# Optimization experiments

Measured on AMD Instinct MI355X. Metric: run time of the kernel, lower is better.

The kernel has to match this reference:

```python
import jax, jax.numpy as jnp
import numpy as np

TOKENS = 1024
IN_W = 512
BLOCK = 256
OUT_W = 512
N_BLOCKS = 64
K = 2


def setup_inputs() -> dict:
    key = jax.random.key(0)
    ks = jax.random.split(key, 8)
    u = lambda k, s: jax.random.uniform(k, s, jnp.float32, -1.0, 1.0)
    return {
        "x": jax.random.normal(ks[0], (TOKENS, IN_W), jnp.float32),
        "noise": jax.random.normal(ks[1], (TOKENS, N_BLOCKS), jnp.float32),
        "w1s": u(ks[2], (N_BLOCKS, IN_W, BLOCK)),
        "b1s": u(ks[3], (N_BLOCKS, BLOCK)),
        "w2s": u(ks[4], (N_BLOCKS, BLOCK, OUT_W)),
        "b2s": u(ks[5], (N_BLOCKS, OUT_W)),
        "mixer": jnp.zeros((IN_W, N_BLOCKS), jnp.float32) + 0.01 * jax.random.normal(ks[6], (IN_W, N_BLOCKS), jnp.float32),
        "noise_controller": jnp.zeros((IN_W, N_BLOCKS), jnp.float32) + 0.01 * jax.random.normal(ks[7], (IN_W, N_BLOCKS), jnp.float32),
        "k": K,
    }


def reference(x, noise, w1s, b1s, w2s, b2s, mixer, noise_controller, k):
    # noisy routing logits: mixer_prod + randn * softplus(noise_prod)
    h_x = x @ mixer + noise * jax.nn.softplus(x @ noise_controller)  # [B, E]
    topk_vals, topk_idx = jax.lax.top_k(h_x, k)                       # [B, K]
    scores = jax.nn.softmax(topk_vals, axis=-1)                       # [B, K]
    # per-token expert weight gather (faithful to index_select semantics)
    gw1 = w1s[topk_idx]  # [B, K, I, H]
    gb1 = b1s[topk_idx]  # [B, K, H]
    gw2 = w2s[topk_idx]  # [B, K, H, O]
    gb2 = b2s[topk_idx]  # [B, K, O]
    v = jax.nn.relu(jnp.einsum('bi,bkih->bkh', x, gw1) + gb1)        # [B, K, H]
    out = jnp.einsum('bkh,bkho->bko', v, gw2) + gb2                   # [B, K, O]
    return jnp.sum(out * scores[..., None], axis=1)                   # [B, O]
```

## Files before the change

kernel.cpp:

```cpp
#include <hip/hip_runtime.h>
#include <math.h>

#define TOKENS    1024
#define IN_W      512
#define BLOCK_H   256
#define OUT_W     512
#define N_EXPERTS 64
#define TOPK      2
#define NSLOTS    (TOKENS * TOPK)
#define LIST_CAP  128
#define T_GRP     12
#define NGRP      4
#define XPAD      520
#define OSPAD     516
#define VPAD      264

__global__ __launch_bounds__(256) void routing_kernel(
    const float* __restrict__ x, const float* __restrict__ noise,
    const float* __restrict__ mixer, const float* __restrict__ noisec,
    float* __restrict__ esc, int* __restrict__ counts, int* __restrict__ lists)
{
    __shared__ float xs[2 * 512];
    __shared__ float pm[2 * 2 * 64];
    __shared__ float pn[2 * 2 * 64];
    const int blk  = blockIdx.x;
    const int tid  = threadIdx.x;
    const int wave = tid >> 6, lane = tid & 63;
    const int tq = wave >> 1;
    const int ih = wave & 1;

    ((float4*)xs)[tid] = ((const float4*)x)[(size_t)blk * 256 + tid];
    __syncthreads();

    float am = 0.f, an = 0.f;
    const float* xp = xs + tq * 512 + ih * 256;
    const float* mp = mixer  + (size_t)(ih * 256) * 64 + lane;
    const float* np = noisec + (size_t)(ih * 256) * 64 + lane;
    #pragma unroll 8
    for (int i = 0; i < 256; ++i) {
        const float xv = xp[i];
        am = fmaf(xv, mp[i * 64], am);
        an = fmaf(xv, np[i * 64], an);
    }
    pm[tq * 128 + ih * 64 + lane] = am;
    pn[tq * 128 + ih * 64 + lane] = an;
    __syncthreads();

    if (tid < 128) {
        const int e = tid & 63, tt = tid >> 6;
        const int t = blk * 2 + tt;
        const float am2 = pm[tt * 128 + e] + pm[tt * 128 + 64 + e];
        const float an2 = pn[tt * 128 + e] + pn[tt * 128 + 64 + e];
        const float sp = fmaxf(an2, 0.f) + log1pf(expf(-fabsf(an2)));
        pm[tt * 128 + e] = am2 + noise[(size_t)t * 64 + e] * sp;
    }
    __syncthreads();

    if (tid < 2) {
        const float* h = pm + tid * 128;
        float b0 = -INFINITY, b1 = -INFINITY;
        int i0 = 0, i1 = 0;
        for (int i = 0; i < N_EXPERTS; ++i) {
            const float v = h[i];
            if (v > b0)      { b1 = b0; i1 = i0; b0 = v; i0 = i; }
            else if (v > b1) { b1 = v; i1 = i; }
        }
        const float z   = expf(b1 - b0);
        const float inv = 1.f / (1.f + z);
        const int t = blk * 2 + tid;
        esc[t * 2 + 0] = inv;
        esc[t * 2 + 1] = z * inv;
        const int p0 = atomicAdd(&counts[i0], 1);
        if (p0 < LIST_CAP) lists[i0 * LIST_CAP + p0] = t * 2 + 0;
        const int p1 = atomicAdd(&counts[i1], 1);
        if (p1 < LIST_CAP) lists[i1 * LIST_CAP + p1] = t * 2 + 1;
    }
}

__global__ __launch_bounds__(1024, 4) void expert_kernel(
    const float* __restrict__ x,
    const float* __restrict__ w1s, const float* __restrict__ b1s,
    const float* __restrict__ w2s, const float* __restrict__ b2s,
    const int* __restrict__ counts, const int* __restrict__ lists,
    const float* __restrict__ esc, float* __restrict__ out)
{
    __shared__ __align__(16) float smem[T_GRP * XPAD];
    __shared__ __align__(16) float vsm[T_GRP * VPAD];
    __shared__ int   slotIds[T_GRP];
    __shared__ float escv[T_GRP];

    const int e  = blockIdx.x;
    const int g  = blockIdx.y;
    const int ne = min(counts[e], LIST_CAP);
    const int tid  = threadIdx.x;
    const int wave = tid >> 6, lane = tid & 63;

    const int cq1  = wave & 3;
    const int tt   = wave >> 2;
    const int c4_1 = cq1 * 16 + (lane & 15);
    const int r1   = lane >> 4;
    const int c4_2 = cq1 * 32 + (lane & 31);
    const int r2   = lane >> 5;
    const int t0   = tt * 3;

    const float4* w1v = (const float4*)(w1s + (size_t)e * IN_W * BLOCK_H);
    const float4* w2v = (const float4*)(w2s + (size_t)e * BLOCK_H * OUT_W);
    const float4* b1v = (const float4*)(b1s + (size_t)e * BLOCK_H);
    const float4* b2v = (const float4*)(b2s + (size_t)e * OUT_W);
    const float4* x4  = (const float4*)x;

    for (int base = g * T_GRP; base < ne; base += NGRP * T_GRP) {
        const int nTok = min(T_GRP, ne - base);
        if (tid < T_GRP) {
            const int s = (tid < nTok) ? lists[e * LIST_CAP + base + tid] : 0;
            slotIds[tid] = s;
            escv[tid]    = esc[s];
        }
        __syncthreads();

        for (int idx = tid; idx < T_GRP * 128; idx += 1024) {
            const int t = idx >> 7, q = idx & 127;
            float4 v = make_float4(0.f, 0.f, 0.f, 0.f);
            if (t < nTok) v = x4[(size_t)(slotIds[t] >> 1) * 128 + q];
            *(float4*)&smem[t * XPAD + q * 4] = v;
        }
        __syncthreads();

        float4 a0 = make_float4(0.f, 0.f, 0.f, 0.f), a1 = a0, a2 = a0;
        {
            const float4* wp = w1v + (size_t)(r1 * 64 + c4_1);
            const float* xb0 = smem + (t0 + 0) * XPAD + r1;
            const float* xb1 = smem + (t0 + 1) * XPAD + r1;
            const float* xb2 = smem + (t0 + 2) * XPAD + r1;
            #pragma unroll 4
            for (int i = 0; i < IN_W; i += 4) {
                const float4 w = wp[(size_t)i * 64];
                const float xv0 = xb0[i], xv1 = xb1[i], xv2 = xb2[i];
                a0.x = fmaf(xv0, w.x, a0.x); a0.y = fmaf(xv0, w.y, a0.y);
                a0.z = fmaf(xv0, w.z, a0.z); a0.w = fmaf(xv0, w.w, a0.w);
                a1.x = fmaf(xv1, w.x, a1.x); a1.y = fmaf(xv1, w.y, a1.y);
                a1.z = fmaf(xv1, w.z, a1.z); a1.w = fmaf(xv1, w.w, a1.w);
                a2.x = fmaf(xv2, w.x, a2.x); a2.y = fmaf(xv2, w.y, a2.y);
                a2.z = fmaf(xv2, w.z, a2.z); a2.w = fmaf(xv2, w.w, a2.w);
            }
        }
        #pragma unroll
        for (int m = 16; m <= 32; m <<= 1) {
            a0.x += __shfl_xor(a0.x, m); a0.y += __shfl_xor(a0.y, m);
            a0.z += __shfl_xor(a0.z, m); a0.w += __shfl_xor(a0.w, m);
            a1.x += __shfl_xor(a1.x, m); a1.y += __shfl_xor(a1.y, m);
            a1.z += __shfl_xor(a1.z, m); a1.w += __shfl_xor(a1.w, m);
            a2.x += __shfl_xor(a2.x, m); a2.y += __shfl_xor(a2.y, m);
            a2.z += __shfl_xor(a2.z, m); a2.w += __shfl_xor(a2.w, m);
        }
        if (lane < 16) {
            const float4 bb = b1v[c4_1];
            float4 r;
            r.x = fmaxf(a0.x + bb.x, 0.f); r.y = fmaxf(a0.y + bb.y, 0.f);
            r.z = fmaxf(a0.z + bb.z, 0.f); r.w = fmaxf(a0.w + bb.w, 0.f);
            *(float4*)&vsm[(t0 + 0) * VPAD + c4_1 * 4] = r;
            r.x = fmaxf(a1.x + bb.x, 0.f); r.y = fmaxf(a1.y + bb.y, 0.f);
            r.z = fmaxf(a1.z + bb.z, 0.f); r.w = fmaxf(a1.w + bb.w, 0.f);
            *(float4*)&vsm[(t0 + 1) * VPAD + c4_1 * 4] = r;
            r.x = fmaxf(a2.x + bb.x, 0.f); r.y = fmaxf(a2.y + bb.y, 0.f);
            r.z = fmaxf(a2.z + bb.z, 0.f); r.w = fmaxf(a2.w + bb.w, 0.f);
            *(float4*)&vsm[(t0 + 2) * VPAD + c4_1 * 4] = r;
        }
        __syncthreads();

        float4 o0 = make_float4(0.f, 0.f, 0.f, 0.f), o1 = o0, o2 = o0;
        {
            const float4* wp2 = w2v + (size_t)(r2 * 128 + c4_2);
            const float* vb0 = vsm + (t0 + 0) * VPAD + r2;
            const float* vb1 = vsm + (t0 + 1) * VPAD + r2;
            const float* vb2 = vsm + (t0 + 2) * VPAD + r2;
            #pragma unroll 4
            for (int h = 0; h < BLOCK_H; h += 2) {
                const float4 w = wp2[(size_t)h * 128];
                const float v0 = vb0[h], v1 = vb1[h], v2 = vb2[h];
                o0.x = fmaf(v0, w.x, o0.x); o0.y = fmaf(v0, w.y, o0.y);
                o0.z = fmaf(v0, w.z, o0.z); o0.w = fmaf(v0, w.w, o0.w);
                o1.x = fmaf(v1, w.x, o1.x); o1.y = fmaf(v1, w.y, o1.y);
                o1.z = fmaf(v1, w.z, o1.z); o1.w = fmaf(v1, w.w, o1.w);
                o2.x = fmaf(v2, w.x, o2.x); o2.y = fmaf(v2, w.y, o2.y);
                o2.z = fmaf(v2, w.z, o2.z); o2.w = fmaf(v2, w.w, o2.w);
            }
        }
        o0.x += __shfl_xor(o0.x, 32); o0.y += __shfl_xor(o0.y, 32);
        o0.z += __shfl_xor(o0.z, 32); o0.w += __shfl_xor(o0.w, 32);
        o1.x += __shfl_xor(o1.x, 32); o1.y += __shfl_xor(o1.y, 32);
        o1.z += __shfl_xor(o1.z, 32); o1.w += __shfl_xor(o1.w, 32);
        o2.x += __shfl_xor(o2.x, 32); o2.y += __shfl_xor(o2.y, 32);
        o2.z += __shfl_xor(o2.z, 32); o2.w += __shfl_xor(o2.w, 32);
        if (lane < 32) {
            *(float4*)&smem[(t0 + 0) * OSPAD + c4_2 * 4] = o0;
            *(float4*)&smem[(t0 + 1) * OSPAD + c4_2 * 4] = o1;
            *(float4*)&smem[(t0 + 2) * OSPAD + c4_2 * 4] = o2;
        }
        __syncthreads();

        for (int idx = tid; idx < T_GRP * 128; idx += 1024) {
            const int t = idx >> 7, q = idx & 127;
            if (t < nTok) {
                const float4 r  = *(const float4*)&smem[t * OSPAD + q * 4];
                const float4 bb = b2v[q];
                const float  sc = escv[t];
                float* o = out + (size_t)(slotIds[t] >> 1) * OUT_W + q * 4;
                atomicAdd(o + 0, (r.x + bb.x) * sc);
                atomicAdd(o + 1, (r.y + bb.y) * sc);
                atomicAdd(o + 2, (r.z + bb.z) * sc);
                atomicAdd(o + 3, (r.w + bb.w) * sc);
            }
        }
        __syncthreads();
    }
}

extern "C" void kernel_launch(void* const* d_in, const int* in_sizes, int n_in,
                              void* d_out, int out_size, void* d_ws, size_t ws_size,
                              hipStream_t stream) {
    const float* x      = (const float*)d_in[0];
    const float* noise  = (const float*)d_in[1];
    const float* w1s    = (const float*)d_in[2];
    const float* b1s    = (const float*)d_in[3];
    const float* w2s    = (const float*)d_in[4];
    const float* b2s    = (const float*)d_in[5];
    const float* mixer  = (const float*)d_in[6];
    const float* noisec = (const float*)d_in[7];
    float* out = (float*)d_out;

    char* ws = (char*)d_ws;
    int*   counts = (int*)ws;                       ws += 256;
    float* esc    = (float*)ws;                     ws += NSLOTS * sizeof(float);
    int*   lists  = (int*)ws;

    hipMemsetAsync(d_out, 0, (size_t)out_size * sizeof(float), stream);
    hipMemsetAsync(counts, 0, 256, stream);

    routing_kernel<<<TOKENS / 2, 256, 0, stream>>>(x, noise, mixer, noisec,
                                                   esc, counts, lists);
    expert_kernel<<<dim3(N_EXPERTS, NGRP), 1024, 0, stream>>>(
        x, w1s, b1s, w2s, b2s, counts, lists, esc, out);
}
```

Measured before the change: 180.7 us.

## Make each wave compute all tokens per expert pass, with templated token-count paths

Each wave now owns a slice of output columns and accumulates every token in the group, so each weight element is loaded once per block instead of once per token-triple wave group. Tokens are interleaved across the NGRP blocks so load is balanced. A template on token count (4/8/12) trims wasted FMAs and staging for sparse experts. The second GEMM's reduced results go straight to global atomics, dropping the output shared-memory stage and one barrier. Larger per-thread accumulator arrays raise register pressure and may lower occupancy.

```diff
diff --git a/kernel.cpp b/kernel.cpp
--- a/kernel.cpp
+++ b/kernel.cpp
@@ -9,10 +9,9 @@
 #define TOPK      2
 #define NSLOTS    (TOKENS * TOPK)
 #define LIST_CAP  128
-#define T_GRP     12
+#define T_CAP     12
 #define NGRP      4
 #define XPAD      520
-#define OSPAD     516
 #define VPAD      264
 
 __global__ __launch_bounds__(256) void routing_kernel(
@@ -77,6 +76,98 @@
     }
 }
 
+__device__ __forceinline__ void red_xor(float4& v, int m) {
+    v.x += __shfl_xor(v.x, m); v.y += __shfl_xor(v.y, m);
+    v.z += __shfl_xor(v.z, m); v.w += __shfl_xor(v.w, m);
+}
+
+template<int T>
+__device__ __forceinline__ void run_pass(
+    int nTok, int wave, int lane,
+    const float4* __restrict__ w1v, const float4* __restrict__ w2v,
+    const float4* __restrict__ b1v, const float4* __restrict__ b2v,
+    const float* __restrict__ xs, float* __restrict__ vsm,
+    const int* __restrict__ slotIds, const float* __restrict__ escv,
+    float* __restrict__ out)
+{
+    {
+        const int c4l = lane & 3, r0 = lane >> 2;
+        float4 acc[T];
+        #pragma unroll
+        for (int t = 0; t < T; ++t) acc[t] = make_float4(0.f, 0.f, 0.f, 0.f);
+        const float4* wp = w1v + (size_t)(r0 * 64 + wave * 4 + c4l);
+        const float*  xb = xs + r0;
+        #pragma unroll 2
+        for (int s = 0; s < 32; ++s) {
+            const float4 w = wp[(size_t)s * 1024];
+            #pragma unroll
+            for (int t = 0; t < T; ++t) {
+                const float xv = xb[t * XPAD + s * 16];
+                acc[t].x = fmaf(xv, w.x, acc[t].x);
+                acc[t].y = fmaf(xv, w.y, acc[t].y);
+                acc[t].z = fmaf(xv, w.z, acc[t].z);
+                acc[t].w = fmaf(xv, w.w, acc[t].w);
+            }
+        }
+        #pragma unroll
+        for (int t = 0; t < T; ++t) {
+            red_xor(acc[t], 4); red_xor(acc[t], 8);
+            red_xor(acc[t], 16); red_xor(acc[t], 32);
+        }
+        if (r0 == 0) {
+            const float4 bb = b1v[wave * 4 + c4l];
+            #pragma unroll
+            for (int t = 0; t < T; ++t) {
+                float4 r;
+                r.x = fmaxf(acc[t].x + bb.x, 0.f);
+                r.y = fmaxf(acc[t].y + bb.y, 0.f);
+                r.z = fmaxf(acc[t].z + bb.z, 0.f);
+                r.w = fmaxf(acc[t].w + bb.w, 0.f);
+                *(float4*)&vsm[t * VPAD + wave * 16 + c4l * 4] = r;
+            }
+        }
+    }
+    __syncthreads();
+
+    {
+        const int c8 = lane & 7, r8 = lane >> 3;
+        float4 acc[T];
+        #pragma unroll
+        for (int t = 0; t < T; ++t) acc[t] = make_float4(0.f, 0.f, 0.f, 0.f);
+        const float4* wp = w2v + (size_t)(r8 * 128 + wave * 8 + c8);
+        const float*  vb = vsm + r8;
+        #pragma unroll 2
+        for (int s = 0; s < 32; ++s) {
+            const float4 w = wp[(size_t)s * 1024];
+            #pragma unroll
+            for (int t = 0; t < T; ++t) {
+                const float vv = vb[t * VPAD + s * 8];
+                acc[t].x = fmaf(vv, w.x, acc[t].x);
+                acc[t].y = fmaf(vv, w.y, acc[t].y);
+                acc[t].z = fmaf(vv, w.z, acc[t].z);
+                acc[t].w = fmaf(vv, w.w, acc[t].w);
+            }
+        }
+        #pragma unroll
+        for (int t = 0; t < T; ++t) {
+            red_xor(acc[t], 8); red_xor(acc[t], 16); red_xor(acc[t], 32);
+        }
+        const float4 bb = b2v[wave * 8 + c8];
+        #pragma unroll
+        for (int t = 0; t < T; ++t) {
+            if ((t & 7) == r8 && t < nTok) {
+                const float sc = escv[t];
+                float* o = out + (size_t)(slotIds[t] >> 1) * OUT_W
+                               + (wave * 8 + c8) * 4;
+                atomicAdd(o + 0, (acc[t].x + bb.x) * sc);
+                atomicAdd(o + 1, (acc[t].y + bb.y) * sc);
+                atomicAdd(o + 2, (acc[t].z + bb.z) * sc);
+                atomicAdd(o + 3, (acc[t].w + bb.w) * sc);
+            }
+        }
+    }
+}
+
 __global__ __launch_bounds__(1024, 4) void expert_kernel(
     const float* __restrict__ x,
     const float* __restrict__ w1s, const float* __restrict__ b1s,
@@ -84,10 +175,10 @@
     const int* __restrict__ counts, const int* __restrict__ lists,
     const float* __restrict__ esc, float* __restrict__ out)
 {
-    __shared__ __align__(16) float smem[T_GRP * XPAD];
-    __shared__ __align__(16) float vsm[T_GRP * VPAD];
-    __shared__ int   slotIds[T_GRP];
-    __shared__ float escv[T_GRP];
+    __shared__ __align__(16) float xs[T_CAP * XPAD];
+    __shared__ __align__(16) float vsm[T_CAP * VPAD];
+    __shared__ int   slotIds[T_CAP];
+    __shared__ float escv[T_CAP];
 
     const int e  = blockIdx.x;
     const int g  = blockIdx.y;
@@ -95,123 +186,38 @@
     const int tid  = threadIdx.x;
     const int wave = tid >> 6, lane = tid & 63;
 
-    const int cq1  = wave & 3;
-    const int tt   = wave >> 2;
-    const int c4_1 = cq1 * 16 + (lane & 15);
-    const int r1   = lane >> 4;
-    const int c4_2 = cq1 * 32 + (lane & 31);
-    const int r2   = lane >> 5;
-    const int t0   = tt * 3;
-
     const float4* w1v = (const float4*)(w1s + (size_t)e * IN_W * BLOCK_H);
     const float4* w2v = (const float4*)(w2s + (size_t)e * BLOCK_H * OUT_W);
     const float4* b1v = (const float4*)(b1s + (size_t)e * BLOCK_H);
     const float4* b2v = (const float4*)(b2s + (size_t)e * OUT_W);
     const float4* x4  = (const float4*)x;
 
-    for (int base = g * T_GRP; base < ne; base += NGRP * T_GRP) {
-        const int nTok = min(T_GRP, ne - base);
-        if (tid < T_GRP) {
-            const int s = (tid < nTok) ? lists[e * LIST_CAP + base + tid] : 0;
+    for (int s0 = g; s0 < ne; s0 += NGRP * T_CAP) {
+        const int nTok  = min(T_CAP, (ne - s0 + NGRP - 1) / NGRP);
+        const int Tpath = (nTok <= 4) ? 4 : (nTok <= 8) ? 8 : 12;
+
+        if (tid < T_CAP) {
+            int s = 0; float sc = 0.f;
+            if (tid < nTok) { s = lists[e * LIST_CAP + s0 + tid * NGRP]; sc = esc[s]; }
             slotIds[tid] = s;
-            escv[tid]    = esc[s];
+            escv[tid]    = sc;
         }
         __syncthreads();
 
-        for (int idx = tid; idx < T_GRP * 128; idx += 1024) {
+        for (int idx = tid; idx < Tpath * 128; idx += 1024) {
             const int t = idx >> 7, q = idx & 127;
             float4 v = make_float4(0.f, 0.f, 0.f, 0.f);
             if (t < nTok) v = x4[(size_t)(slotIds[t] >> 1) * 128 + q];
-            *(float4*)&smem[t * XPAD + q * 4] = v;
+            *(float4*)&xs[t * XPAD + q * 4] = v;
         }
         __syncthreads();
 
-        float4 a0 = make_float4(0.f, 0.f, 0.f, 0.f), a1 = a0, a2 = a0;
-        {
-            const float4* wp = w1v + (size_t)(r1 * 64 + c4_1);
-            const float* xb0 = smem + (t0 + 0) * XPAD + r1;
-            const float* xb1 = smem + (t0 + 1) * XPAD + r1;
-            const float* xb2 = smem + (t0 + 2) * XPAD + r1;
-            #pragma unroll 4
-            for (int i = 0; i < IN_W; i += 4) {
-                const float4 w = wp[(size_t)i * 64];
-                const float xv0 = xb0[i], xv1 = xb1[i], xv2 = xb2[i];
-                a0.x = fmaf(xv0, w.x, a0.x); a0.y = fmaf(xv0, w.y, a0.y);
-                a0.z = fmaf(xv0, w.z, a0.z); a0.w = fmaf(xv0, w.w, a0.w);
-                a1.x = fmaf(xv1, w.x, a1.x); a1.y = fmaf(xv1, w.y, a1.y);
-                a1.z = fmaf(xv1, w.z, a1.z); a1.w = fmaf(xv1, w.w, a1.w);
-                a2.x = fmaf(xv2, w.x, a2.x); a2.y = fmaf(xv2, w.y, a2.y);
-                a2.z = fmaf(xv2, w.z, a2.z); a2.w = fmaf(xv2, w.w, a2.w);
-            }
-        }
-        #pragma unroll
-        for (int m = 16; m <= 32; m <<= 1) {
-            a0.x += __shfl_xor(a0.x, m); a0.y += __shfl_xor(a0.y, m);
-            a0.z += __shfl_xor(a0.z, m); a0.w += __shfl_xor(a0.w, m);
-            a1.x += __shfl_xor(a1.x, m); a1.y += __shfl_xor(a1.y, m);
-            a1.z += __shfl_xor(a1.z, m); a1.w += __shfl_xor(a1.w, m);
-            a2.x += __shfl_xor(a2.x, m); a2.y += __shfl_xor(a2.y, m);
-            a2.z += __shfl_xor(a2.z, m); a2.w += __shfl_xor(a2.w, m);
-        }
-        if (lane < 16) {
-            const float4 bb = b1v[c4_1];
-            float4 r;
-            r.x = fmaxf(a0.x + bb.x, 0.f); r.y = fmaxf(a0.y + bb.y, 0.f);
-            r.z = fmaxf(a0.z + bb.z, 0.f); r.w = fmaxf(a0.w + bb.w, 0.f);
-            *(float4*)&vsm[(t0 + 0) * VPAD + c4_1 * 4] = r;
-            r.x = fmaxf(a1.x + bb.x, 0.f); r.y = fmaxf(a1.y + bb.y, 0.f);
-            r.z = fmaxf(a1.z + bb.z, 0.f); r.w = fmaxf(a1.w + bb.w, 0.f);
-            *(float4*)&vsm[(t0 + 1) * VPAD + c4_1 * 4] = r;
-            r.x = fmaxf(a2.x + bb.x, 0.f); r.y = fmaxf(a2.y + bb.y, 0.f);
-            r.z = fmaxf(a2.z + bb.z, 0.f); r.w = fmaxf(a2.w + bb.w, 0.f);
-            *(float4*)&vsm[(t0 + 2) * VPAD + c4_1 * 4] = r;
-        }
-        __syncthreads();
-
-        float4 o0 = make_float4(0.f, 0.f, 0.f, 0.f), o1 = o0, o2 = o0;
-        {
-            const float4* wp2 = w2v + (size_t)(r2 * 128 + c4_2);
-            const float* vb0 = vsm + (t0 + 0) * VPAD + r2;
-            const float* vb1 = vsm + (t0 + 1) * VPAD + r2;
-            const float* vb2 = vsm + (t0 + 2) * VPAD + r2;
-            #pragma unroll 4
-            for (int h = 0; h < BLOCK_H; h += 2) {
-                const float4 w = wp2[(size_t)h * 128];
-                const float v0 = vb0[h], v1 = vb1[h], v2 = vb2[h];
-                o0.x = fmaf(v0, w.x, o0.x); o0.y = fmaf(v0, w.y, o0.y);
-                o0.z = fmaf(v0, w.z, o0.z); o0.w = fmaf(v0, w.w, o0.w);
-                o1.x = fmaf(v1, w.x, o1.x); o1.y = fmaf(v1, w.y, o1.y);
-                o1.z = fmaf(v1, w.z, o1.z); o1.w = fmaf(v1, w.w, o1.w);
-                o2.x = fmaf(v2, w.x, o2.x); o2.y = fmaf(v2, w.y, o2.y);
-                o2.z = fmaf(v2, w.z, o2.z); o2.w = fmaf(v2, w.w, o2.w);
-            }
-        }
-        o0.x += __shfl_xor(o0.x, 32); o0.y += __shfl_xor(o0.y, 32);
-        o0.z += __shfl_xor(o0.z, 32); o0.w += __shfl_xor(o0.w, 32);
-        o1.x += __shfl_xor(o1.x, 32); o1.y += __shfl_xor(o1.y, 32);
-        o1.z += __shfl_xor(o1.z, 32); o1.w += __shfl_xor(o1.w, 32);
-        o2.x += __shfl_xor(o2.x, 32); o2.y += __shfl_xor(o2.y, 32);
-        o2.z += __shfl_xor(o2.z, 32); o2.w += __shfl_xor(o2.w, 32);
-        if (lane < 32) {
-            *(float4*)&smem[(t0 + 0) * OSPAD + c4_2 * 4] = o0;
-            *(float4*)&smem[(t0 + 1) * OSPAD + c4_2 * 4] = o1;
-            *(float4*)&smem[(t0 + 2) * OSPAD + c4_2 * 4] = o2;
-        }
-        __syncthreads();
-
-        for (int idx = tid; idx < T_GRP * 128; idx += 1024) {
-            const int t = idx >> 7, q = idx & 127;
-            if (t < nTok) {
-                const float4 r  = *(const float4*)&smem[t * OSPAD + q * 4];
-                const float4 bb = b2v[q];
-                const float  sc = escv[t];
-                float* o = out + (size_t)(slotIds[t] >> 1) * OUT_W + q * 4;
-                atomicAdd(o + 0, (r.x + bb.x) * sc);
-                atomicAdd(o + 1, (r.y + bb.y) * sc);
-                atomicAdd(o + 2, (r.z + bb.z) * sc);
-                atomicAdd(o + 3, (r.w + bb.w) * sc);
-            }
-        }
+        if (nTok <= 4)
+            run_pass<4>(nTok, wave, lane, w1v, w2v, b1v, b2v, xs, vsm, slotIds, escv, out);
+        else if (nTok <= 8)
+            run_pass<8>(nTok, wave, lane, w1v, w2v, b1v, b2v, xs, vsm, slotIds, escv, out);
+        else
+            run_pass<12>(nTok, wave, lane, w1v, w2v, b1v, b2v, xs, vsm, slotIds, escv, out);
         __syncthreads();
     }
 }
```

After: 172.5 us. -4.5%, faster.
